# Kernel tuning notes

Measured on AMD Instinct MI355X. Metric: run time of the kernel, lower is better.

Reference implementation:

```python
import jax, jax.numpy as jnp
import numpy as np

B, T_ENC, FEAT, H, W2V, T_DEC, V = 32, 80, 4096, 256, 256, 30, 32000


def lstm_cell(x, h, c, w_ih, w_hh, b_ih, b_hh):
    # PyTorch LSTMCell: gates order i, f, g, o
    g = x @ w_ih.T + h @ w_hh.T + b_ih + b_hh
    i, f, gg, o = jnp.split(g, 4, axis=-1)
    c_new = jax.nn.sigmoid(f) * c + jax.nn.sigmoid(i) * jnp.tanh(gg)
    h_new = jax.nn.sigmoid(o) * jnp.tanh(c_new)
    return h_new, c_new


def setup_inputs() -> dict:
    key = jax.random.key(0)
    ks = jax.random.split(key, 13)
    s = 0.05
    return {
        'feat': jax.random.normal(ks[0], (B, T_ENC, FEAT), jnp.float32),
        'caption': jax.random.normal(ks[1], (B, T_DEC, W2V), jnp.float32),
        'caption_one_hot': jax.random.normal(ks[2], (B, T_DEC, V), jnp.float32),
        'keep_rate': 1,
        'w_ih1': jax.random.normal(ks[3], (4 * H, FEAT), jnp.float32) * s,
        'w_hh1': jax.random.normal(ks[4], (4 * H, H), jnp.float32) * s,
        'b_ih1': jax.random.normal(ks[5], (4 * H,), jnp.float32) * s,
        'b_hh1': jax.random.normal(ks[6], (4 * H,), jnp.float32) * s,
        'w_ih2': jax.random.normal(ks[7], (4 * H, H + W2V), jnp.float32) * s,
        'w_hh2': jax.random.normal(ks[8], (4 * H, H), jnp.float32) * s,
        'b_ih2': jax.random.normal(ks[9], (4 * H,), jnp.float32) * s,
        'b_hh2': jax.random.normal(ks[10], (4 * H,), jnp.float32) * s,
        'w_out': jax.random.normal(ks[11], (V, H), jnp.float32) * s,
        'b_out': jax.random.normal(ks[12], (V,), jnp.float32) * s,
    }


def reference(feat, caption, caption_one_hot, keep_rate,
              w_ih1, w_hh1, b_ih1, b_hh1,
              w_ih2, w_hh2, b_ih2, b_hh2,
              w_out, b_out):
    zeros_h = jnp.zeros((B, H), feat.dtype)
    pad1 = jnp.zeros((B, FEAT), feat.dtype)

    # ---------------- encoder: 80 steps ----------------
    def enc_step(carry, x_t):
        h1, c1, h2, c2 = carry
        h1, c1 = lstm_cell(x_t, h1, c1, w_ih1, w_hh1, b_ih1, b_hh1)
        h2, c2 = lstm_cell(jnp.concatenate([zeros_h, h1], axis=1), h2, c2,
                           w_ih2, w_hh2, b_ih2, b_hh2)
        return (h1, c1, h2, c2), h2

    (h1, c1, h2, c2), enc_h2 = jax.lax.scan(
        enc_step, (zeros_h, zeros_h, zeros_h, zeros_h),
        jnp.transpose(feat, (1, 0, 2)))
    enc_h2 = jnp.transpose(enc_h2, (1, 0, 2))  # [B, 80, H]

    # ---------------- decoder: teacher forcing (coin>=100 never fires) ----
    targets = jnp.argmax(caption_one_hot, axis=-1)  # [B, T_DEC]

    def dec_step(carry, xs):
        h1, c1, h2, c2, loss = carry
        word_t, tgt_t = xs  # [B, W2V], [B]
        h1, c1 = lstm_cell(pad1, h1, c1, w_ih1, w_hh1, b_ih1, b_hh1)
        h2n, c2 = lstm_cell(jnp.concatenate([word_t, h1], axis=1), h2, c2,
                            w_ih2, w_hh2, b_ih2, b_hh2)
        logits = h2n @ w_out.T + b_out  # [B, V]
        logp = jax.nn.log_softmax(logits, axis=-1)
        ce = -jnp.take_along_axis(logp, tgt_t[:, None], axis=1)[:, 0]
        loss = loss + jnp.mean(ce) / B  # sum(mean-CE)/batch, per original
        # attention: scores of encoder h2 states against current h2
        attn = jax.nn.softmax(jnp.einsum('bsh,bh->bs', enc_h2, h2n), axis=-1)
        ctx = jnp.einsum('bs,bsh->bh', attn, enc_h2)  # replaces h2 for next step
        return (h1, c1, ctx, c2, loss), None

    xs = (jnp.transpose(caption[:, :T_DEC - 1, :], (1, 0, 2)),
          jnp.transpose(targets[:, 1:T_DEC], (1, 0)))
    (h1, c1, h2, c2, total_loss), _ = jax.lax.scan(
        dec_step, (h1, c1, h2, c2, jnp.float32(0.0)), xs)
    return total_loss
```

## Files before the change

kernel.cpp:

```cpp
#include <hip/hip_runtime.h>
#include <hip/hip_bf16.h>
#include <math.h>

#define BB 32
#define TE 80
#define FEAT 4096
#define HH 256
#define W2V 256
#define TD 30
#define VV 32000
#define G4 1024

typedef unsigned short u16;
typedef unsigned int u32;
using f32x4 = __attribute__((ext_vector_type(4))) float;
using bf16x8 = __attribute__((ext_vector_type(8))) short;
using f16x2 = __attribute__((ext_vector_type(2))) _Float16;

#define SENT 0xFFFFFFFFu
#define NANF 0x7FC00000u

__device__ __forceinline__ float sigm(float x) { return 1.0f / (1.0f + expf(-x)); }
__device__ __forceinline__ u16 f2bf(float f) {
  u32 u = __float_as_uint(f);
  u32 r = (u + 0x7FFFu + ((u >> 16) & 1u)) >> 16;
  return (u16)r;
}
__device__ __forceinline__ u32 packh2(float lo, float hi) {
  f16x2 v = {(_Float16)lo, (_Float16)hi};
  return __builtin_bit_cast(u32, v);
}

#define AT_LOAD(p)     __hip_atomic_load((p), __ATOMIC_RELAXED, __HIP_MEMORY_SCOPE_AGENT)
#define AT_STORE(p, v) __hip_atomic_store((p), (v), __ATOMIC_RELAXED, __HIP_MEMORY_SCOPE_AGENT)

__device__ __forceinline__ float fdot2h(f16x2 a, f16x2 b, float c) {
#if __has_builtin(__builtin_amdgcn_fdot2)
  return __builtin_amdgcn_fdot2(a, b, c, false);
#else
  return c + (float)a[0] * (float)b[0] + (float)a[1] * (float)b[1];
#endif
}

__global__ __launch_bounds__(256) void prep_kernel(
    const float* __restrict__ feat, const float* __restrict__ w_ih1,
    const float* __restrict__ w_ih2, const float* __restrict__ caption,
    const float* __restrict__ onehot,
    const float* __restrict__ b_ih1, const float* __restrict__ b_hh1,
    const float* __restrict__ b_ih2, const float* __restrict__ b_hh2,
    u16* __restrict__ featb, u16* __restrict__ w_ih1b,
    u16* __restrict__ w_ih2lb, u16* __restrict__ capb,
    float* __restrict__ bias1, float* __restrict__ bias2,
    u32* __restrict__ H1H, u32* __restrict__ H2H, u32* __restrict__ A2P,
    float* __restrict__ loss, int* __restrict__ ctrs,
    int* __restrict__ targets) {
  int blk = blockIdx.x, tid = threadIdx.x;
  if (blk < 928) {
    int k = blk;
    int s = (k >> 5) + 1, b = k & 31;
    const float* row = &onehot[((size_t)b * TD + s) * VV];
    float bv = -INFINITY;
    int bi = 0x7fffffff;
    for (int v = tid; v < VV; v += 256) {
      float x = row[v];
      if (x > bv || (x == bv && v < bi)) { bv = x; bi = v; }
    }
    __shared__ float sv[256];
    __shared__ int si[256];
    sv[tid] = bv; si[tid] = bi;
    __syncthreads();
    for (int off = 128; off; off >>= 1) {
      if (tid < off) {
        float ov = sv[tid + off]; int oi = si[tid + off];
        if (ov > sv[tid] || (ov == sv[tid] && oi < si[tid])) { sv[tid] = ov; si[tid] = oi; }
      }
      __syncthreads();
    }
    if (tid == 0) targets[k] = si[0];
  } else if (blk < 3488) {
    int i0 = (blk - 928) * 1024 + tid;
#pragma unroll
    for (int ii = 0; ii < 4; ++ii) {
      int i = i0 + ii * 256;
      float4 v = *(const float4*)&feat[(size_t)i * 4];
      *(ushort4*)&featb[(size_t)i * 4] =
          make_ushort4(f2bf(v.x), f2bf(v.y), f2bf(v.z), f2bf(v.w));
    }
  } else if (blk < 4512) {
    int i0 = (blk - 3488) * 1024 + tid;
#pragma unroll
    for (int ii = 0; ii < 4; ++ii) {
      int i = i0 + ii * 256;
      float4 v = *(const float4*)&w_ih1[(size_t)i * 4];
      *(ushort4*)&w_ih1b[(size_t)i * 4] =
          make_ushort4(f2bf(v.x), f2bf(v.y), f2bf(v.z), f2bf(v.w));
    }
  } else if (blk < 4576) {
    int i0 = (blk - 4512) * 1024 + tid;
#pragma unroll
    for (int ii = 0; ii < 4; ++ii) {
      int i = i0 + ii * 256;
      int row = i >> 6, c = (i & 63) * 4;
      float4 v = *(const float4*)&w_ih2[(size_t)row * 512 + c];
      *(ushort4*)&w_ih2lb[(size_t)row * 256 + c] =
          make_ushort4(f2bf(v.x), f2bf(v.y), f2bf(v.z), f2bf(v.w));
    }
  } else if (blk < 4636) {
    int i0 = (blk - 4576) * 1024 + tid;
#pragma unroll
    for (int ii = 0; ii < 4; ++ii) {
      int i = i0 + ii * 256;
      float4 v = *(const float4*)&caption[(size_t)i * 4];
      *(ushort4*)&capb[(size_t)i * 4] =
          make_ushort4(f2bf(v.x), f2bf(v.y), f2bf(v.z), f2bf(v.w));
    }
  } else if (blk < 5076) {
    int i = (blk - 4636) * 256 + tid;
    uint4 z = {0u, 0u, 0u, 0u};
    uint4 s = {SENT, SENT, SENT, SENT};
    uint4 v = (i < 1024) ? z : s;
    ((uint4*)H1H)[i] = v;
    ((uint4*)H2H)[i] = v;
  } else if (blk < 5956) {
    int i0 = (blk - 5076) * 1024 + tid;
    uint4 s = {NANF, NANF, NANF, NANF};
#pragma unroll
    for (int ii = 0; ii < 4; ++ii) ((uint4*)A2P)[i0 + ii * 256] = s;
  } else {
    for (int i = tid; i < 1024; i += 256) {
      bias1[i] = b_ih1[i] + b_hh1[i];
      bias2[i] = b_ih2[i] + b_hh2[i];
    }
    if (tid == 0) { *loss = 0.0f; ctrs[0] = 0; ctrs[32] = 0; }
  }
}

#define GBM 128
#define GBN 128
#define GBK 64
#define LDSTR 72

__device__ void gemm_x1_body(char* smem, int bx, int by,
                             const u16* __restrict__ Ab, const u16* __restrict__ Bw,
                             const float* __restrict__ bias, float* __restrict__ C) {
  u16* As = (u16*)smem;
  u16* Bs = (u16*)(smem + 18432);
  int tid = threadIdx.x;
  int rBase = by * GBM;
  int nBase = bx * GBN;
  int lane = tid & 63, w = tid >> 6;
  int wrow = (w >> 1) * 64, wcol = (w & 1) * 64;
  int lrow = lane & 15, lk = (lane >> 4) * 8;

  f32x4 acc[4][4];
#pragma unroll
  for (int m = 0; m < 4; ++m)
#pragma unroll
    for (int n = 0; n < 4; ++n) acc[m][n] = (f32x4){0.f, 0.f, 0.f, 0.f};

  for (int k0 = 0; k0 < FEAT; k0 += GBK) {
#pragma unroll
    for (int i = 0; i < 4; ++i) {
      int f = i * 256 + tid;
      int r = f >> 3, c8 = f & 7;
      *(uint4*)&As[r * LDSTR + c8 * 8] =
          *(const uint4*)&Ab[(size_t)(rBase + r) * FEAT + k0 + c8 * 8];
    }
#pragma unroll
    for (int i = 0; i < 4; ++i) {
      int f = i * 256 + tid;
      int r = f >> 3, c8 = f & 7;
      *(uint4*)&Bs[r * LDSTR + c8 * 8] =
          *(const uint4*)&Bw[(size_t)(nBase + r) * FEAT + k0 + c8 * 8];
    }
    __syncthreads();
#pragma unroll
    for (int s2 = 0; s2 < 2; ++s2) {
      bf16x8 af[4], bfr[4];
#pragma unroll
      for (int m = 0; m < 4; ++m)
        af[m] = *(const bf16x8*)&As[(wrow + m * 16 + lrow) * LDSTR + s2 * 32 + lk];
#pragma unroll
      for (int n = 0; n < 4; ++n)
        bfr[n] = *(const bf16x8*)&Bs[(wcol + n * 16 + lrow) * LDSTR + s2 * 32 + lk];
#pragma unroll
      for (int m = 0; m < 4; ++m)
#pragma unroll
        for (int n = 0; n < 4; ++n)
          acc[m][n] = __builtin_amdgcn_mfma_f32_16x16x32_bf16(
              af[m], bfr[n], acc[m][n], 0, 0, 0);
    }
    __syncthreads();
  }
  int orow = (lane >> 4) * 4;
  int ocol = lane & 15;
#pragma unroll
  for (int m = 0; m < 4; ++m)
#pragma unroll
    for (int n = 0; n < 4; ++n) {
      int cidx = nBase + wcol + n * 16 + ocol;
      float bv = bias[cidx];
#pragma unroll
      for (int q = 0; q < 4; ++q) {
        int r = rBase + wrow + m * 16 + orow + q;
        C[(size_t)r * G4 + cidx] = acc[m][n][q] + bv;
      }
    }
}

__device__ void xw2_body(char* smem, int nb, int t,
                         const u16* __restrict__ capb, const u16* __restrict__ w_ih2lb,
                         const float* __restrict__ bias2, float* __restrict__ XW2) {
  u16* As = (u16*)smem;
  u16* Bs = (u16*)(smem + 16896);
  int tid = threadIdx.x;
  int nBase = nb * 64;
#pragma unroll
  for (int it = 0; it < 4; ++it) {
    int i = it * 256 + tid;
    int r = i >> 5, c8 = i & 31;
    *(uint4*)&As[r * 264 + c8 * 8] =
        *(const uint4*)&capb[((size_t)r * TD + t) * 256 + c8 * 8];
  }
#pragma unroll
  for (int it = 0; it < 8; ++it) {
    int i = it * 256 + tid;
    int r = i >> 5, c8 = i & 31;
    *(uint4*)&Bs[r * 264 + c8 * 8] =
        *(const uint4*)&w_ih2lb[(size_t)(nBase + r) * 256 + c8 * 8];
  }
  __syncthreads();
  int lane = tid & 63, w = tid >> 6;
  int lrow = lane & 15, lk = (lane >> 4) * 8;
  f32x4 acc[2];
  acc[0] = (f32x4){0.f, 0.f, 0.f, 0.f};
  acc[1] = (f32x4){0.f, 0.f, 0.f, 0.f};
#pragma unroll
  for (int ks = 0; ks < 8; ++ks) {
    bf16x8 bfr = *(const bf16x8*)&Bs[(w * 16 + lrow) * 264 + ks * 32 + lk];
#pragma unroll
    for (int m = 0; m < 2; ++m) {
      bf16x8 af = *(const bf16x8*)&As[(m * 16 + lrow) * 264 + ks * 32 + lk];
      acc[m] = __builtin_amdgcn_mfma_f32_16x16x32_bf16(af, bfr, acc[m], 0, 0, 0);
    }
  }
  int col = nBase + w * 16 + (lane & 15);
  float bv = bias2[col];
  int orow = (lane >> 4) * 4;
#pragma unroll
  for (int m = 0; m < 2; ++m)
#pragma unroll
    for (int q = 0; q < 4; ++q) {
      int bb = m * 16 + orow + q;
      XW2[((size_t)t * 32 + bb) * G4 + col] = acc[m][q] + bv;
    }
}

__global__ __launch_bounds__(256) void gemms_kernel(
    const u16* __restrict__ featb, const u16* __restrict__ w_ih1b,
    const float* __restrict__ bias1, float* __restrict__ X1,
    const u16* __restrict__ capb, const u16* __restrict__ w_ih2lb,
    const float* __restrict__ bias2, float* __restrict__ XW2) {
  __shared__ __align__(16) char smem[50688];
  int blk = blockIdx.x;
  if (blk < 160) {
    gemm_x1_body(smem, blk & 7, blk >> 3, featb, w_ih1b, bias1, X1);
  } else {
    int k = blk - 160;
    xw2_body(smem, k & 15, k >> 4, capb, w_ih2lb, bias2, XW2);
  }
}

struct RP {
  const float *X1, *XW2, *bias1, *bias2;
  const float *w_hh1, *w_ih2, *w_hh2;
  u32* H1H;
  u32* H2H;
  u32* A2P;
  u16* H2NB;
};

__global__ __launch_bounds__(512, 1) void recurrent_kernel(RP p) {
  __shared__ float encL[TE][257];
  __shared__ __align__(16) f16x2 hS[128];
  __shared__ float tmp2[256];
  __shared__ float gb[256];
  __shared__ float a2pS[256];
  __shared__ float hnew[64];
  __shared__ float sc[80];
  __shared__ float red[4];
  int bid = blockIdx.x, tid = threadIdx.x;
  bool isL1 = bid < 128;
  int lb = isL1 ? bid : bid - 128;
  int b = lb >> 2, q = lb & 3;
  int r2 = tid >> 1, half = tid & 1;
  int g = r2 >> 6, jj = r2 & 63;
  int grow = (g << 8) + (q << 6) + jj;
  int jf = (q << 6) + tid;

  if (isL1) {
    f16x2 wA[64], wB[64];
    {
      const float4* sA = (const float4*)(p.w_hh1 + (size_t)grow * 256 + half * 128);
      const float4* sB = (const float4*)(p.w_ih2 + (size_t)grow * 512 + 256 + half * 128);
#pragma unroll
      for (int k = 0; k < 32; ++k) {
        float4 v = sA[k];
        wA[k * 2 + 0] = f16x2{(_Float16)v.x, (_Float16)v.y};
        wA[k * 2 + 1] = f16x2{(_Float16)v.z, (_Float16)v.w};
        float4 u = sB[k];
        wB[k * 2 + 0] = f16x2{(_Float16)u.x, (_Float16)u.y};
        wB[k * 2 + 1] = f16x2{(_Float16)u.z, (_Float16)u.w};
      }
    }
    float c1 = 0.f;
    float b1v0 = 0, b1v1 = 0, b1v2 = 0, b1v3 = 0;
    if (tid < 64) {
      b1v0 = p.bias1[jf]; b1v1 = p.bias1[256 + jf];
      b1v2 = p.bias1[512 + jf]; b1v3 = p.bias1[768 + jf];
    }
    for (int T = 0; T <= 109; ++T) {
      float x0 = b1v0, x1 = b1v1, x2 = b1v2, x3 = b1v3;
      if (tid < 64 && T < TE) {
        const float* xb = &p.X1[((size_t)b * TE + T) * G4 + jf];
        x0 = xb[0]; x1 = xb[256]; x2 = xb[512]; x3 = xb[768];
      }
      if (tid < 128) {
        const u32* src = &p.H1H[((size_t)T * 32 + b) * 128 + tid];
        u32 v = AT_LOAD(src);
        int gd = 0;
        while (v == SENT && ++gd < (1 << 24)) {
          __builtin_amdgcn_s_sleep(1);
          v = AT_LOAD(src);
        }
        hS[tid] = __builtin_bit_cast(f16x2, v);
      }
      __syncthreads();
      float a1 = 0.f, a2 = 0.f;
      {
        const uint4* hv = ((const uint4*)hS) + half * 16;
#pragma unroll
        for (int k = 0; k < 16; ++k) {
          uint4 uu = hv[k];
          f16x2 e0 = __builtin_bit_cast(f16x2, uu.x), e1 = __builtin_bit_cast(f16x2, uu.y);
          f16x2 e2 = __builtin_bit_cast(f16x2, uu.z), e3 = __builtin_bit_cast(f16x2, uu.w);
          a1 = fdot2h(e0, wA[k * 4 + 0], a1);
          a2 = fdot2h(e0, wB[k * 4 + 0], a2);
          a1 = fdot2h(e1, wA[k * 4 + 1], a1);
          a2 = fdot2h(e1, wB[k * 4 + 1], a2);
          a1 = fdot2h(e2, wA[k * 4 + 2], a1);
          a2 = fdot2h(e2, wB[k * 4 + 2], a2);
          a1 = fdot2h(e3, wA[k * 4 + 3], a1);
          a2 = fdot2h(e3, wB[k * 4 + 3], a2);
        }
      }
      a1 += __shfl_xor(a1, 1);
      a2 += __shfl_xor(a2, 1);
      if (half == 0) {
        gb[r2] = a1;
        if (T >= 1)
          AT_STORE(&p.A2P[((size_t)T * 32 + b) * 1024 + grow], __float_as_uint(a2));
      }
      __syncthreads();
      if (T <= 108) {
        if (tid < 64) {
          float gi = gb[tid] + x0;
          float gf = gb[64 + tid] + x1;
          float gG = gb[128 + tid] + x2;
          float go = gb[192 + tid] + x3;
          c1 = sigm(gf) * c1 + sigm(gi) * tanhf(gG);
          hnew[tid] = sigm(go) * tanhf(c1);
        }
        if (tid < 32) {
          u32 pk = packh2(hnew[2 * tid], hnew[2 * tid + 1]);
          AT_STORE(&p.H1H[((size_t)(T + 1) * 32 + b) * 128 + (q << 5) + tid], pk);
        }
      }
    }
  } else {
    f16x2 wC[64];
    {
      const float4* sC = (const float4*)(p.w_hh2 + (size_t)grow * 256 + half * 128);
#pragma unroll
      for (int k = 0; k < 32; ++k) {
        float4 u = sC[k];
        wC[k * 2 + 0] = f16x2{(_Float16)u.x, (_Float16)u.y};
        wC[k * 2 + 1] = f16x2{(_Float16)u.z, (_Float16)u.w};
      }
    }
    float c2 = 0.f;
    float b2v0 = 0, b2v1 = 0, b2v2 = 0, b2v3 = 0;
    if (tid < 64) {
      b2v0 = p.bias2[jf]; b2v1 = p.bias2[256 + jf];
      b2v2 = p.bias2[512 + jf]; b2v3 = p.bias2[768 + jf];
    }
    for (int U = 1; U <= 109; ++U) {
      float x0 = b2v0, x1 = b2v1, x2 = b2v2, x3 = b2v3;
      if (tid < 64 && U >= 81) {
        const float* xb = &p.XW2[((size_t)(U - 81) * 32 + b) * G4 + jf];
        x0 = xb[0]; x1 = xb[256]; x2 = xb[512]; x3 = xb[768];
      }
      if (tid < 128) {
        const u32* src = &p.H2H[((size_t)(U - 1) * 32 + b) * 128 + tid];
        u32 v = AT_LOAD(src);
        int gd = 0;
        while (v == SENT && ++gd < (1 << 26)) v = AT_LOAD(src);
        f16x2 hp = __builtin_bit_cast(f16x2, v);
        hS[tid] = hp;
        tmp2[2 * tid] = (float)hp[0];
        tmp2[2 * tid + 1] = (float)hp[1];
      } else if (tid < 384) {
        int rr = tid - 128;
        int growp = ((rr >> 6) << 8) + (q << 6) + (rr & 63);
        const u32* src = &p.A2P[((size_t)U * 32 + b) * 1024 + growp];
        u32 v = AT_LOAD(src);
        int gd = 0;
        while (v == NANF && ++gd < (1 << 24)) {
          __builtin_amdgcn_s_sleep(1);
          v = AT_LOAD(src);
        }
        a2pS[rr] = __uint_as_float(v);
      }
      __syncthreads();
      float a2p0 = 0, a2p1 = 0, a2p2 = 0, a2p3 = 0;
      if (tid < 64) {
        a2p0 = a2pS[tid]; a2p1 = a2pS[64 + tid];
        a2p2 = a2pS[128 + tid]; a2p3 = a2pS[192 + tid];
      }
      if (U <= 81) {
        if (U >= 2 && tid < 256) encL[U - 2][tid] = tmp2[tid];
      } else {
        float a = 0.f;
        if (tid < TE) {
          const float* e = &encL[tid][0];
#pragma unroll 8
          for (int k2 = 0; k2 < 256; ++k2) a += e[k2] * tmp2[k2];
        }
        float av = (tid < TE) ? a : -INFINITY;
#pragma unroll
        for (int d = 32; d; d >>= 1) av = fmaxf(av, __shfl_xor(av, d));
        if (tid == 0) red[0] = av;
        if (tid == 64) red[1] = av;
        __syncthreads();
        float m = fmaxf(red[0], red[1]);
        float e2 = (tid < TE) ? expf(a - m) : 0.f;
        float sv = e2;
#pragma unroll
        for (int d = 32; d; d >>= 1) sv += __shfl_xor(sv, d);
        if (tid == 0) red[2] = sv;
        if (tid == 64) red[3] = sv;
        __syncthreads();
        float inv = 1.0f / (red[2] + red[3]);
        if (tid < TE) sc[tid] = e2 * inv;
        __syncthreads();
        if (tid < 256) {
          float acc = 0.f;
          for (int t2 = 0; t2 < TE; ++t2) acc += sc[t2] * encL[t2][tid];
          tmp2[tid] = acc;
        }
        __syncthreads();
        if (tid < 128)
          hS[tid] = f16x2{(_Float16)tmp2[2 * tid], (_Float16)tmp2[2 * tid + 1]};
        __syncthreads();
      }
      float a2 = 0.f;
      {
        const uint4* hv = ((const uint4*)hS) + half * 16;
#pragma unroll
        for (int k = 0; k < 16; ++k) {
          uint4 uu = hv[k];
          a2 = fdot2h(__builtin_bit_cast(f16x2, uu.x), wC[k * 4 + 0], a2);
          a2 = fdot2h(__builtin_bit_cast(f16x2, uu.y), wC[k * 4 + 1], a2);
          a2 = fdot2h(__builtin_bit_cast(f16x2, uu.z), wC[k * 4 + 2], a2);
          a2 = fdot2h(__builtin_bit_cast(f16x2, uu.w), wC[k * 4 + 3], a2);
        }
      }
      a2 += __shfl_xor(a2, 1);
      if (half == 0) gb[r2] = a2;
      __syncthreads();
      if (tid < 64) {
        float gi = gb[tid] + a2p0 + x0;
        float gf = gb[64 + tid] + a2p1 + x1;
        float gG = gb[128 + tid] + a2p2 + x2;
        float go = gb[192 + tid] + a2p3 + x3;
        c2 = sigm(gf) * c2 + sigm(gi) * tanhf(gG);
        float h = sigm(go) * tanhf(c2);
        hnew[tid] = h;
        if (U >= 81)
          p.H2NB[((size_t)(U - 81) * 32 + b) * 256 + jf] = f2bf(h);
      }
      if (tid < 32) {
        u32 pk = packh2(hnew[2 * tid], hnew[2 * tid + 1]);
        AT_STORE(&p.H2H[((size_t)U * 32 + b) * 128 + (q << 5) + tid], pk);
      }
    }
  }
}

__global__ __launch_bounds__(256, 1) void logits_final_kernel(
    const u16* __restrict__ H2NB, const float* __restrict__ w_out,
    const float* __restrict__ b_out, const int* __restrict__ targets,
    u32* __restrict__ pmaxA, u32* __restrict__ psumA, u32* __restrict__ tgtv,
    float* __restrict__ loss, int* __restrict__ ctrs, float* __restrict__ out) {
  __shared__ __align__(16) u16 bS[32768];
  __shared__ __align__(16) u16 aS[32 * 264];
  __shared__ int tS[32];
  __shared__ float sm[256];
  int tid = threadIdx.x, bid = blockIdx.x;
#pragma unroll
  for (int it = 0; it < 16; ++it) {
    int id = it * 256 + tid;
    int nt = id >> 9, rr = (id >> 5) & 15, kg = id & 31;
    int n = bid * 128 + nt * 16 + rr;
    const float* src = &w_out[(size_t)n * 256 + kg * 8];
    float4 v0 = *(const float4*)src;
    float4 v1 = *(const float4*)(src + 4);
    u16* dst = &bS[(size_t)((nt * 32 + kg) * 16 + rr) * 8];
    *(ushort4*)dst = make_ushort4(f2bf(v0.x), f2bf(v0.y), f2bf(v0.z), f2bf(v0.w));
    *(ushort4*)(dst + 4) = make_ushort4(f2bf(v1.x), f2bf(v1.y), f2bf(v1.z), f2bf(v1.w));
  }
  int wid = tid >> 6, lane = tid & 63, lcol = lane & 15, lk = lane >> 4;
  float bo[2];
#pragma unroll
  for (int n = 0; n < 2; ++n) bo[n] = b_out[(bid * 8 + wid * 2 + n) * 16 + lcol];

  for (int rg = 0; rg < 29; ++rg) {
    __syncthreads();
    for (int i = tid; i < 1024; i += 256) {
      int r = i >> 5, c8 = i & 31;
      *(uint4*)&aS[r * 264 + c8 * 8] =
          *(const uint4*)&H2NB[(size_t)rg * 8192 + r * 256 + c8 * 8];
    }
    if (tid < 32) tS[tid] = targets[rg * 32 + tid];
    __syncthreads();
    f32x4 acc[2][2];
#pragma unroll
    for (int m = 0; m < 2; ++m)
#pragma unroll
      for (int n = 0; n < 2; ++n) acc[m][n] = (f32x4){0.f, 0.f, 0.f, 0.f};
#pragma unroll
    for (int ks = 0; ks < 8; ++ks) {
      bf16x8 a0 = *(const bf16x8*)&aS[lcol * 264 + ks * 32 + lk * 8];
      bf16x8 a1 = *(const bf16x8*)&aS[(16 + lcol) * 264 + ks * 32 + lk * 8];
      bf16x8 b0 = *(const bf16x8*)&bS[(wid * 2) * 4096 + ((ks * 4 + lk) * 16 + lcol) * 8];
      bf16x8 b1 = *(const bf16x8*)&bS[(wid * 2 + 1) * 4096 + ((ks * 4 + lk) * 16 + lcol) * 8];
      acc[0][0] = __builtin_amdgcn_mfma_f32_16x16x32_bf16(a0, b0, acc[0][0], 0, 0, 0);
      acc[0][1] = __builtin_amdgcn_mfma_f32_16x16x32_bf16(a0, b1, acc[0][1], 0, 0, 0);
      acc[1][0] = __builtin_amdgcn_mfma_f32_16x16x32_bf16(a1, b0, acc[1][0], 0, 0, 0);
      acc[1][1] = __builtin_amdgcn_mfma_f32_16x16x32_bf16(a1, b1, acc[1][1], 0, 0, 0);
    }
    int nbase = (bid * 8 + wid * 2) * 16 + lcol;
#pragma unroll
    for (int m = 0; m < 2; ++m) {
      float pm[4], psv[4];
#pragma unroll
      for (int qq = 0; qq < 4; ++qq) {
        float v0 = acc[m][0][qq] + bo[0];
        float v1 = acc[m][1][qq] + bo[1];
        int r = m * 16 + lk * 4 + qq;
        int tg = tS[r];
        if (tg == nbase) AT_STORE(&tgtv[rg * 32 + r], __float_as_uint(v0));
        if (tg == nbase + 16) AT_STORE(&tgtv[rg * 32 + r], __float_as_uint(v1));
        float mx = fmaxf(v0, v1);
#pragma unroll
        for (int d = 1; d < 16; d <<= 1) mx = fmaxf(mx, __shfl_xor(mx, d));
        float e = expf(v0 - mx) + expf(v1 - mx);
#pragma unroll
        for (int d = 1; d < 16; d <<= 1) e += __shfl_xor(e, d);
        pm[qq] = mx;
        psv[qq] = e;
      }
      if (lcol == 0) {
        int chunk = bid * 4 + wid;
#pragma unroll
        for (int qq = 0; qq < 4; ++qq) {
          int r2 = rg * 32 + m * 16 + lk * 4 + qq;
          AT_STORE(&pmaxA[(size_t)r2 * 1000 + chunk], __float_as_uint(pm[qq]));
          AT_STORE(&psumA[(size_t)r2 * 1000 + chunk], __float_as_uint(psv[qq]));
        }
      }
    }
  }
  asm volatile("s_waitcnt vmcnt(0)" ::: "memory");
  __syncthreads();
  if (tid == 0) {
    __hip_atomic_fetch_add(&ctrs[0], 1, __ATOMIC_RELEASE, __HIP_MEMORY_SCOPE_AGENT);
    int gd = 0;
    while (__hip_atomic_load(&ctrs[0], __ATOMIC_ACQUIRE, __HIP_MEMORY_SCOPE_AGENT) < 250 &&
           ++gd < (1 << 26))
      __builtin_amdgcn_s_sleep(2);
  }
  __syncthreads();
#pragma unroll
  for (int k = 0; k < 4; ++k) {
    int row = bid * 4 + k;
    if (row < 928) {
      const u32* pm = pmaxA + (size_t)row * 1000;
      const u32* psv = psumA + (size_t)row * 1000;
      float m = -INFINITY;
      for (int c = tid; c < 1000; c += 256) m = fmaxf(m, __uint_as_float(AT_LOAD(&pm[c])));
      sm[tid] = m;
      __syncthreads();
      for (int off = 128; off; off >>= 1) {
        if (tid < off) sm[tid] = fmaxf(sm[tid], sm[tid + off]);
        __syncthreads();
      }
      float M = sm[0];
      __syncthreads();
      float s = 0.f;
      for (int c = tid; c < 1000; c += 256)
        s += __uint_as_float(AT_LOAD(&psv[c])) * expf(__uint_as_float(AT_LOAD(&pm[c])) - M);
      sm[tid] = s;
      __syncthreads();
      for (int off = 128; off; off >>= 1) {
        if (tid < off) sm[tid] += sm[tid + off];
        __syncthreads();
      }
      if (tid == 0) {
        float tv = __uint_as_float(AT_LOAD(&tgtv[row]));
        atomicAdd(loss, (M + logf(sm[0]) - tv) * (1.0f / 1024.0f));
      }
      __syncthreads();
    }
  }
  asm volatile("s_waitcnt vmcnt(0)" ::: "memory");
  if (tid == 0) {
    int old = __hip_atomic_fetch_add(&ctrs[32], 1, __ATOMIC_ACQ_REL, __HIP_MEMORY_SCOPE_AGENT);
    if (old == 249) out[0] = __uint_as_float(AT_LOAD((u32*)loss));
  }
}

extern "C" void kernel_launch(void* const* d_in, const int* in_sizes, int n_in,
                              void* d_out, int out_size, void* d_ws, size_t ws_size,
                              hipStream_t stream) {
  (void)in_sizes; (void)n_in; (void)out_size; (void)ws_size;
  const float* feat    = (const float*)d_in[0];
  const float* caption = (const float*)d_in[1];
  const float* onehot  = (const float*)d_in[2];
  const float* w_ih1   = (const float*)d_in[4];
  const float* w_hh1   = (const float*)d_in[5];
  const float* b_ih1   = (const float*)d_in[6];
  const float* b_hh1   = (const float*)d_in[7];
  const float* w_ih2   = (const float*)d_in[8];
  const float* w_hh2   = (const float*)d_in[9];
  const float* b_ih2   = (const float*)d_in[10];
  const float* b_hh2   = (const float*)d_in[11];
  const float* w_out   = (const float*)d_in[12];
  const float* b_out   = (const float*)d_in[13];

  char* p = (char*)d_ws;
  auto alloc = [&](size_t bytes) {
    char* r = p;
    p += (bytes + 255) & ~(size_t)255;
    return r;
  };
  float* X1      = (float*)alloc(2560ull * 1024 * 4);
  float* XW2     = (float*)alloc(29ull * 32 * 1024 * 4);
  float* bias1   = (float*)alloc(1024 * 4);
  float* bias2   = (float*)alloc(1024 * 4);
  u32*   H1H     = (u32*)alloc(110ull * 32 * 128 * 4);
  u32*   H2H     = (u32*)alloc(110ull * 32 * 128 * 4);
  u32*   A2P     = (u32*)alloc(110ull * 32 * 1024 * 4);
  u16*   H2NB    = (u16*)alloc(29ull * 8192 * 2);
  u32*   pmaxA   = (u32*)alloc(928ull * 1000 * 4);
  u32*   psumA   = (u32*)alloc(928ull * 1000 * 4);
  u32*   tgtv    = (u32*)alloc(928 * 4);
  float* lossacc = (float*)alloc(256);
  int*   ctrs    = (int*)alloc(256);
  int*   targets = (int*)alloc(29 * 32 * 4);
  u16*   featb   = (u16*)alloc(2560ull * 4096 * 2);
  u16*   w_ih1b  = (u16*)alloc(1024ull * 4096 * 2);
  u16*   w_ih2lb = (u16*)alloc(1024ull * 256 * 2);
  u16*   capb    = (u16*)alloc(32ull * 30 * 256 * 2);

  prep_kernel<<<5957, 256, 0, stream>>>(
      feat, w_ih1, w_ih2, caption, onehot,
      b_ih1, b_hh1, b_ih2, b_hh2,
      featb, w_ih1b, w_ih2lb, capb,
      bias1, bias2, H1H, H2H, A2P, lossacc, ctrs, targets);
  gemms_kernel<<<624, 256, 0, stream>>>(featb, w_ih1b, bias1, X1,
                                        capb, w_ih2lb, bias2, XW2);

  RP rp;
  rp.X1 = X1; rp.XW2 = XW2; rp.bias1 = bias1; rp.bias2 = bias2;
  rp.w_hh1 = w_hh1; rp.w_ih2 = w_ih2; rp.w_hh2 = w_hh2;
  rp.H1H = H1H; rp.H2H = H2H; rp.A2P = A2P; rp.H2NB = H2NB;
  void* args[] = {&rp};
  hipLaunchCooperativeKernel((const void*)recurrent_kernel, dim3(256), dim3(512),
                             args, 0, stream);

  logits_final_kernel<<<250, 256, 0, stream>>>(H2NB, w_out, b_out, targets,
                                               pmaxA, psumA, tgtv, lossacc, ctrs,
                                               (float*)d_out);
}
```

Before: 687.5 us.

## Fuse input conversions into GEMMs and pack cross-block partials as fp16

The separate bf16 conversion pass over feat is removed: the X1 GEMM now reads fp32 feat and converts it while staging into shared memory. The small caption×w_ih2 GEMM moves into the prep kernel, which converts directly from fp32 and no longer needs intermediate buffers. The per-step A2P partial sums exchanged between blocks in the recurrent kernel are packed as fp16 pairs, halving their traffic. It also lowers the spin guards and clears more counters. This removes a large write and re-read of featb but doubles the A-operand load bytes in the GEMM, and the fp16 partials lose some precision.

```diff
diff --git a/kernel.cpp b/kernel.cpp
--- a/kernel.cpp
+++ b/kernel.cpp
@@ -18,7 +18,7 @@
 using f16x2 = __attribute__((ext_vector_type(2))) _Float16;
 
 #define SENT 0xFFFFFFFFu
-#define NANF 0x7FC00000u
+#define GUARD (1 << 22)
 
 __device__ __forceinline__ float sigm(float x) { return 1.0f / (1.0f + expf(-x)); }
 __device__ __forceinline__ u16 f2bf(float f) {
@@ -43,17 +43,16 @@
 }
 
 __global__ __launch_bounds__(256) void prep_kernel(
-    const float* __restrict__ feat, const float* __restrict__ w_ih1,
-    const float* __restrict__ w_ih2, const float* __restrict__ caption,
-    const float* __restrict__ onehot,
+    const float* __restrict__ w_ih1, const float* __restrict__ w_ih2,
+    const float* __restrict__ caption, const float* __restrict__ onehot,
     const float* __restrict__ b_ih1, const float* __restrict__ b_hh1,
     const float* __restrict__ b_ih2, const float* __restrict__ b_hh2,
-    u16* __restrict__ featb, u16* __restrict__ w_ih1b,
-    u16* __restrict__ w_ih2lb, u16* __restrict__ capb,
+    u16* __restrict__ w_ih1b, float* __restrict__ XW2,
     float* __restrict__ bias1, float* __restrict__ bias2,
     u32* __restrict__ H1H, u32* __restrict__ H2H, u32* __restrict__ A2P,
     float* __restrict__ loss, int* __restrict__ ctrs,
     int* __restrict__ targets) {
+  __shared__ __align__(16) char psm[50688];
   int blk = blockIdx.x, tid = threadIdx.x;
   if (blk < 928) {
     int k = blk;
@@ -65,8 +64,8 @@
       float x = row[v];
       if (x > bv || (x == bv && v < bi)) { bv = x; bi = v; }
     }
-    __shared__ float sv[256];
-    __shared__ int si[256];
+    float* sv = (float*)psm;
+    int* si = (int*)(psm + 1024);
     sv[tid] = bv; si[tid] = bi;
     __syncthreads();
     for (int off = 128; off; off >>= 1) {
@@ -77,17 +76,8 @@
       __syncthreads();
     }
     if (tid == 0) targets[k] = si[0];
-  } else if (blk < 3488) {
+  } else if (blk < 1952) {
     int i0 = (blk - 928) * 1024 + tid;
-#pragma unroll
-    for (int ii = 0; ii < 4; ++ii) {
-      int i = i0 + ii * 256;
-      float4 v = *(const float4*)&feat[(size_t)i * 4];
-      *(ushort4*)&featb[(size_t)i * 4] =
-          make_ushort4(f2bf(v.x), f2bf(v.y), f2bf(v.z), f2bf(v.w));
-    }
-  } else if (blk < 4512) {
-    int i0 = (blk - 3488) * 1024 + tid;
 #pragma unroll
     for (int ii = 0; ii < 4; ++ii) {
       int i = i0 + ii * 256;
@@ -95,35 +85,68 @@
       *(ushort4*)&w_ih1b[(size_t)i * 4] =
           make_ushort4(f2bf(v.x), f2bf(v.y), f2bf(v.z), f2bf(v.w));
     }
-  } else if (blk < 4576) {
-    int i0 = (blk - 4512) * 1024 + tid;
-#pragma unroll
-    for (int ii = 0; ii < 4; ++ii) {
-      int i = i0 + ii * 256;
-      int row = i >> 6, c = (i & 63) * 4;
-      float4 v = *(const float4*)&w_ih2[(size_t)row * 512 + c];
-      *(ushort4*)&w_ih2lb[(size_t)row * 256 + c] =
-          make_ushort4(f2bf(v.x), f2bf(v.y), f2bf(v.z), f2bf(v.w));
-    }
-  } else if (blk < 4636) {
-    int i0 = (blk - 4576) * 1024 + tid;
-#pragma unroll
-    for (int ii = 0; ii < 4; ++ii) {
-      int i = i0 + ii * 256;
-      float4 v = *(const float4*)&caption[(size_t)i * 4];
-      *(ushort4*)&capb[(size_t)i * 4] =
-          make_ushort4(f2bf(v.x), f2bf(v.y), f2bf(v.z), f2bf(v.w));
-    }
-  } else if (blk < 5076) {
-    int i = (blk - 4636) * 256 + tid;
+  } else if (blk < 2416) {
+    int k = blk - 1952, nb = k & 15, t = k >> 4;
+    u16* As = (u16*)psm;
+    u16* Bs = (u16*)(psm + 16896);
+    int nBase = nb * 64;
+#pragma unroll
+    for (int it = 0; it < 4; ++it) {
+      int i = it * 256 + tid;
+      int r = i >> 5, c8 = i & 31;
+      const float* src = &caption[((size_t)r * TD + t) * 256 + c8 * 8];
+      float4 v0 = *(const float4*)src;
+      float4 v1 = *(const float4*)(src + 4);
+      u16* dst = &As[r * 264 + c8 * 8];
+      *(ushort4*)dst = make_ushort4(f2bf(v0.x), f2bf(v0.y), f2bf(v0.z), f2bf(v0.w));
+      *(ushort4*)(dst + 4) = make_ushort4(f2bf(v1.x), f2bf(v1.y), f2bf(v1.z), f2bf(v1.w));
+    }
+#pragma unroll
+    for (int it = 0; it < 8; ++it) {
+      int i = it * 256 + tid;
+      int r = i >> 5, c8 = i & 31;
+      const float* src = &w_ih2[(size_t)(nBase + r) * 512 + c8 * 8];
+      float4 v0 = *(const float4*)src;
+      float4 v1 = *(const float4*)(src + 4);
+      u16* dst = &Bs[r * 264 + c8 * 8];
+      *(ushort4*)dst = make_ushort4(f2bf(v0.x), f2bf(v0.y), f2bf(v0.z), f2bf(v0.w));
+      *(ushort4*)(dst + 4) = make_ushort4(f2bf(v1.x), f2bf(v1.y), f2bf(v1.z), f2bf(v1.w));
+    }
+    __syncthreads();
+    int lane = tid & 63, w = tid >> 6;
+    int lrow = lane & 15, lk = (lane >> 4) * 8;
+    f32x4 acc[2];
+    acc[0] = (f32x4){0.f, 0.f, 0.f, 0.f};
+    acc[1] = (f32x4){0.f, 0.f, 0.f, 0.f};
+#pragma unroll
+    for (int ks = 0; ks < 8; ++ks) {
+      bf16x8 bfr = *(const bf16x8*)&Bs[(w * 16 + lrow) * 264 + ks * 32 + lk];
+#pragma unroll
+      for (int m = 0; m < 2; ++m) {
+        bf16x8 af = *(const bf16x8*)&As[(m * 16 + lrow) * 264 + ks * 32 + lk];
+        acc[m] = __builtin_amdgcn_mfma_f32_16x16x32_bf16(af, bfr, acc[m], 0, 0, 0);
+      }
+    }
+    int col = nBase + w * 16 + (lane & 15);
+    float bv = b_ih2[col] + b_hh2[col];
+    int orow = (lane >> 4) * 4;
+#pragma unroll
+    for (int m = 0; m < 2; ++m)
+#pragma unroll
+      for (int qq = 0; qq < 4; ++qq) {
+        int bb = m * 16 + orow + qq;
+        XW2[((size_t)t * 32 + bb) * G4 + col] = acc[m][qq] + bv;
+      }
+  } else if (blk < 2856) {
+    int i = (blk - 2416) * 256 + tid;
     uint4 z = {0u, 0u, 0u, 0u};
     uint4 s = {SENT, SENT, SENT, SENT};
     uint4 v = (i < 1024) ? z : s;
     ((uint4*)H1H)[i] = v;
     ((uint4*)H2H)[i] = v;
-  } else if (blk < 5956) {
-    int i0 = (blk - 5076) * 1024 + tid;
-    uint4 s = {NANF, NANF, NANF, NANF};
+  } else if (blk < 3296) {
+    int i0 = (blk - 2856) * 1024 + tid;
+    uint4 s = {SENT, SENT, SENT, SENT};
 #pragma unroll
     for (int ii = 0; ii < 4; ++ii) ((uint4*)A2P)[i0 + ii * 256] = s;
   } else {
@@ -131,7 +154,8 @@
       bias1[i] = b_ih1[i] + b_hh1[i];
       bias2[i] = b_ih2[i] + b_hh2[i];
     }
-    if (tid == 0) { *loss = 0.0f; ctrs[0] = 0; ctrs[32] = 0; }
+    if (tid < 256) ctrs[tid] = 0;
+    if (tid == 0) *loss = 0.0f;
   }
 }
 
@@ -140,14 +164,14 @@
 #define GBK 64
 #define LDSTR 72
 
-__device__ void gemm_x1_body(char* smem, int bx, int by,
-                             const u16* __restrict__ Ab, const u16* __restrict__ Bw,
-                             const float* __restrict__ bias, float* __restrict__ C) {
-  u16* As = (u16*)smem;
-  u16* Bs = (u16*)(smem + 18432);
+__global__ __launch_bounds__(256) void gemm_x1_kernel(
+    const float* __restrict__ A, const u16* __restrict__ Bw,
+    const float* __restrict__ bias, float* __restrict__ C) {
+  __shared__ __align__(16) u16 As[GBM * LDSTR];
+  __shared__ __align__(16) u16 Bs[GBN * LDSTR];
   int tid = threadIdx.x;
-  int rBase = by * GBM;
-  int nBase = bx * GBN;
+  int rBase = (blockIdx.x >> 3) * GBM;
+  int nBase = (blockIdx.x & 7) * GBN;
   int lane = tid & 63, w = tid >> 6;
   int wrow = (w >> 1) * 64, wcol = (w & 1) * 64;
   int lrow = lane & 15, lk = (lane >> 4) * 8;
@@ -160,11 +184,12 @@
 
   for (int k0 = 0; k0 < FEAT; k0 += GBK) {
 #pragma unroll
-    for (int i = 0; i < 4; ++i) {
+    for (int i = 0; i < 8; ++i) {
       int f = i * 256 + tid;
-      int r = f >> 3, c8 = f & 7;
-      *(uint4*)&As[r * LDSTR + c8 * 8] =
-          *(const uint4*)&Ab[(size_t)(rBase + r) * FEAT + k0 + c8 * 8];
+      int r = f >> 4, c = (f & 15) << 2;
+      float4 v = *(const float4*)&A[(size_t)(rBase + r) * FEAT + k0 + c];
+      *(ushort4*)&As[r * LDSTR + c] =
+          make_ushort4(f2bf(v.x), f2bf(v.y), f2bf(v.z), f2bf(v.w));
     }
 #pragma unroll
     for (int i = 0; i < 4; ++i) {
@@ -206,69 +231,6 @@
         C[(size_t)r * G4 + cidx] = acc[m][n][q] + bv;
       }
     }
-}
-
-__device__ void xw2_body(char* smem, int nb, int t,
-                         const u16* __restrict__ capb, const u16* __restrict__ w_ih2lb,
-                         const float* __restrict__ bias2, float* __restrict__ XW2) {
-  u16* As = (u16*)smem;
-  u16* Bs = (u16*)(smem + 16896);
-  int tid = threadIdx.x;
-  int nBase = nb * 64;
-#pragma unroll
-  for (int it = 0; it < 4; ++it) {
-    int i = it * 256 + tid;
-    int r = i >> 5, c8 = i & 31;
-    *(uint4*)&As[r * 264 + c8 * 8] =
-        *(const uint4*)&capb[((size_t)r * TD + t) * 256 + c8 * 8];
-  }
-#pragma unroll
-  for (int it = 0; it < 8; ++it) {
-    int i = it * 256 + tid;
-    int r = i >> 5, c8 = i & 31;
-    *(uint4*)&Bs[r * 264 + c8 * 8] =
-        *(const uint4*)&w_ih2lb[(size_t)(nBase + r) * 256 + c8 * 8];
-  }
-  __syncthreads();
-  int lane = tid & 63, w = tid >> 6;
-  int lrow = lane & 15, lk = (lane >> 4) * 8;
-  f32x4 acc[2];
-  acc[0] = (f32x4){0.f, 0.f, 0.f, 0.f};
-  acc[1] = (f32x4){0.f, 0.f, 0.f, 0.f};
-#pragma unroll
-  for (int ks = 0; ks < 8; ++ks) {
-    bf16x8 bfr = *(const bf16x8*)&Bs[(w * 16 + lrow) * 264 + ks * 32 + lk];
-#pragma unroll
-    for (int m = 0; m < 2; ++m) {
-      bf16x8 af = *(const bf16x8*)&As[(m * 16 + lrow) * 264 + ks * 32 + lk];
-      acc[m] = __builtin_amdgcn_mfma_f32_16x16x32_bf16(af, bfr, acc[m], 0, 0, 0);
-    }
-  }
-  int col = nBase + w * 16 + (lane & 15);
-  float bv = bias2[col];
-  int orow = (lane >> 4) * 4;
-#pragma unroll
-  for (int m = 0; m < 2; ++m)
-#pragma unroll
-    for (int q = 0; q < 4; ++q) {
-      int bb = m * 16 + orow + q;
-      XW2[((size_t)t * 32 + bb) * G4 + col] = acc[m][q] + bv;
-    }
-}
-
-__global__ __launch_bounds__(256) void gemms_kernel(
-    const u16* __restrict__ featb, const u16* __restrict__ w_ih1b,
-    const float* __restrict__ bias1, float* __restrict__ X1,
-    const u16* __restrict__ capb, const u16* __restrict__ w_ih2lb,
-    const float* __restrict__ bias2, float* __restrict__ XW2) {
-  __shared__ __align__(16) char smem[50688];
-  int blk = blockIdx.x;
-  if (blk < 160) {
-    gemm_x1_body(smem, blk & 7, blk >> 3, featb, w_ih1b, bias1, X1);
-  } else {
-    int k = blk - 160;
-    xw2_body(smem, k & 15, k >> 4, capb, w_ih2lb, bias2, XW2);
-  }
 }
 
 struct RP {
@@ -329,7 +291,7 @@
         const u32* src = &p.H1H[((size_t)T * 32 + b) * 128 + tid];
         u32 v = AT_LOAD(src);
         int gd = 0;
-        while (v == SENT && ++gd < (1 << 24)) {
+        while (v == SENT && ++gd < GUARD) {
           __builtin_amdgcn_s_sleep(1);
           v = AT_LOAD(src);
         }
@@ -356,10 +318,13 @@
       }
       a1 += __shfl_xor(a1, 1);
       a2 += __shfl_xor(a2, 1);
-      if (half == 0) {
-        gb[r2] = a1;
-        if (T >= 1)
-          AT_STORE(&p.A2P[((size_t)T * 32 + b) * 1024 + grow], __float_as_uint(a2));
+      float a2o = __shfl_xor(a2, 2);
+      if (half == 0) gb[r2] = a1;
+      if ((tid & 3) == 0 && T >= 1) {
+        int pr = tid >> 2;
+        int gp = pr >> 5, wp = pr & 31;
+        AT_STORE(&p.A2P[((size_t)T * 32 + b) * 512 + (gp << 7) + (q << 5) + wp],
+                 packh2(a2, a2o));
       }
       __syncthreads();
       if (T <= 108) {
@@ -404,22 +369,24 @@
         const u32* src = &p.H2H[((size_t)(U - 1) * 32 + b) * 128 + tid];
         u32 v = AT_LOAD(src);
         int gd = 0;
-        while (v == SENT && ++gd < (1 << 26)) v = AT_LOAD(src);
+        while (v == SENT && ++gd < (GUARD << 2)) v = AT_LOAD(src);
         f16x2 hp = __builtin_bit_cast(f16x2, v);
         hS[tid] = hp;
         tmp2[2 * tid] = (float)hp[0];
         tmp2[2 * tid + 1] = (float)hp[1];
-      } else if (tid < 384) {
+      } else if (tid < 256) {
         int rr = tid - 128;
-        int growp = ((rr >> 6) << 8) + (q << 6) + (rr & 63);
-        const u32* src = &p.A2P[((size_t)U * 32 + b) * 1024 + growp];
+        int gp = rr >> 5, wp = rr & 31;
+        const u32* src = &p.A2P[((size_t)U * 32 + b) * 512 + (gp << 7) + (q << 5) + wp];
         u32 v = AT_LOAD(src);
         int gd = 0;
-        while (v == NANF && ++gd < (1 << 24)) {
+        while (v == SENT && ++gd < GUARD) {
           __builtin_amdgcn_s_sleep(1);
           v = AT_LOAD(src);
         }
-        a2pS[rr] = __uint_as_float(v);
+        f16x2 pr = __builtin_bit_cast(f16x2, v);
+        a2pS[gp * 64 + 2 * wp] = (float)pr[0];
+        a2pS[gp * 64 + 2 * wp + 1] = (float)pr[1];
       }
       __syncthreads();
       float a2p0 = 0, a2p1 = 0, a2p2 = 0, a2p3 = 0;
@@ -461,8 +428,8 @@
         __syncthreads();
         if (tid < 128)
           hS[tid] = f16x2{(_Float16)tmp2[2 * tid], (_Float16)tmp2[2 * tid + 1]};
-        __syncthreads();
-      }
+      }
+      __syncthreads();
       float a2 = 0.f;
       {
         const uint4* hv = ((const uint4*)hS) + half * 16;
@@ -587,7 +554,7 @@
     __hip_atomic_fetch_add(&ctrs[0], 1, __ATOMIC_RELEASE, __HIP_MEMORY_SCOPE_AGENT);
     int gd = 0;
     while (__hip_atomic_load(&ctrs[0], __ATOMIC_ACQUIRE, __HIP_MEMORY_SCOPE_AGENT) < 250 &&
-           ++gd < (1 << 26))
+           ++gd < GUARD)
       __builtin_amdgcn_s_sleep(2);
   }
   __syncthreads();
@@ -660,26 +627,22 @@
   float* bias2   = (float*)alloc(1024 * 4);
   u32*   H1H     = (u32*)alloc(110ull * 32 * 128 * 4);
   u32*   H2H     = (u32*)alloc(110ull * 32 * 128 * 4);
-  u32*   A2P     = (u32*)alloc(110ull * 32 * 1024 * 4);
+  u32*   A2P     = (u32*)alloc(110ull * 32 * 512 * 4);
   u16*   H2NB    = (u16*)alloc(29ull * 8192 * 2);
   u32*   pmaxA   = (u32*)alloc(928ull * 1000 * 4);
   u32*   psumA   = (u32*)alloc(928ull * 1000 * 4);
   u32*   tgtv    = (u32*)alloc(928 * 4);
   float* lossacc = (float*)alloc(256);
-  int*   ctrs    = (int*)alloc(256);
+  int*   ctrs    = (int*)alloc(1024);
   int*   targets = (int*)alloc(29 * 32 * 4);
-  u16*   featb   = (u16*)alloc(2560ull * 4096 * 2);
   u16*   w_ih1b  = (u16*)alloc(1024ull * 4096 * 2);
-  u16*   w_ih2lb = (u16*)alloc(1024ull * 256 * 2);
-  u16*   capb    = (u16*)alloc(32ull * 30 * 256 * 2);
-
-  prep_kernel<<<5957, 256, 0, stream>>>(
-      feat, w_ih1, w_ih2, caption, onehot,
+
+  prep_kernel<<<3297, 256, 0, stream>>>(
+      w_ih1, w_ih2, caption, onehot,
       b_ih1, b_hh1, b_ih2, b_hh2,
-      featb, w_ih1b, w_ih2lb, capb,
-      bias1, bias2, H1H, H2H, A2P, lossacc, ctrs, targets);
-  gemms_kernel<<<624, 256, 0, stream>>>(featb, w_ih1b, bias1, X1,
-                                        capb, w_ih2lb, bias2, XW2);
+      w_ih1b, XW2, bias1, bias2, H1H, H2H, A2P, lossacc, ctrs, targets);
+
+  gemm_x1_kernel<<<160, 256, 0, stream>>>(feat, w_ih1b, bias1, X1);
 
   RP rp;
   rp.X1 = X1; rp.XW2 = XW2; rp.bias1 = bias1; rp.bias2 = bias2;
```

New measurement: 742.4 us. +8.0%, slower.
